# Kernel optimization log

Hardware: AMD Instinct MI355X
Metric: run time of the kernel (lower is better)

The kernel has to match this reference:

```python
import jax, jax.numpy as jnp
import numpy as np

KH = KW = 21          # kernel_size
DIL = 1               # dilation
Q_SCALE = 1e10        # floor-quantization scale from the original module


def setup_inputs() -> dict:
    key = jax.random.key(0)
    # (B, N, C, H, W) with N = num_input = 2
    inputs = jax.random.normal(key, (4, 2, 128, 128, 128), dtype=jnp.float32)
    return {"inputs": inputs}


def reference(inputs):
    B, N, C, H, W = inputs.shape
    Rh, Rw = (KH // 2) * DIL, (KW // 2) * DIL  # max displacement per axis

    # floor quantization with straight-through gradient (matches detach trick)
    s = jnp.float32(Q_SCALE)
    q = jax.lax.stop_gradient(jnp.floor(inputs * s) / s - inputs) + inputs

    src = q[:, :-1]        # (B, N-1, C, H, W)
    target = q[:, -1]      # (B, C, H, W)

    # zero padding == grid_sample padding_mode='zeros', nearest + integer offsets
    tp = jnp.pad(target, ((0, 0), (0, 0), (Rh, Rh), (Rw, Rw)))

    # row-major enumeration of displacements (dy, dx); slice start = R + d
    dy = jnp.arange(KH, dtype=jnp.int32) * DIL   # 0 .. 2*Rh
    dx = jnp.arange(KW, dtype=jnp.int32) * DIL
    starts = jnp.stack(jnp.meshgrid(dy, dx, indexing='ij'), axis=-1).reshape(-1, 2)  # (K, 2)

    def step(carry, st):
        # shifted[h, w] = target[h + dy, w + dx] with zeros outside
        sh = jax.lax.dynamic_slice(tp, (0, 0, st[0], st[1]), (B, C, H, W))
        # elementwise multiply + channel mean -> (B, N-1, H, W)
        return carry, jnp.mean(src * sh[:, None], axis=-3)

    _, ys = jax.lax.scan(step, None, starts)          # (K, B, N-1, H, W)
    out = jnp.moveaxis(ys, 0, 1)                      # (B, K, N-1, H, W)
    return out.reshape(B, KH * KW * (N - 1), H, W)    # stack dim=1 then flatten(1,2)
```

## Files before the change

kernel.cpp:

```cpp
#include <hip/hip_runtime.h>

#define HH 128
#define WW 128
#define CCH 128
#define NKD 21
#define RAD 10
#define HPAD 148
#define ROWH 40
#define CH_HALVES (148 * ROWH)
#define CH_BYTES  (CH_HALVES * 2)
#define IMG_HALVES (4 * CH_HALVES)

typedef _Float16 f16x8 __attribute__((ext_vector_type(8)));
typedef float    f32x4 __attribute__((ext_vector_type(4)));
typedef __fp16   h2f   __attribute__((ext_vector_type(2)));

union PK { uint4 u; h2f h[4]; };

__global__ __launch_bounds__(256)
void pack_tgt(const float* __restrict__ in, __fp16* __restrict__ img) {
    int n = blockIdx.x;
    int b = n / HPAD, i = n - b * HPAD;
    int tid = threadIdx.x;
    uint4* gi = (uint4*)(img + (size_t)n * IMG_HALVES);
    if (i < RAD || i > 137) {
        uint4 z = make_uint4(0, 0, 0, 0);
#pragma unroll
        for (int k = 0; k < 11; ++k) gi[k * 256 + tid] = z;
        if (tid < 144) gi[11 * 256 + tid] = z;
        return;
    }
    __shared__ __align__(16) char sraw[4 * CH_BYTES];
    {
        uint4 z = make_uint4(0, 0, 0, 0);
        uint4* sp = (uint4*)sraw;
#pragma unroll
        for (int k = 0; k < 11; ++k) sp[k * 256 + tid] = z;
        if (tid < 144) sp[11 * 256 + tid] = z;
    }
    __syncthreads();
    const float* tg = in + (size_t)(b * 2 + 1) * CCH * HH * WW + (size_t)(i - RAD) * WW;
    int w = tid & 127, half = tid >> 7;
    int p = w + RAD;
#pragma unroll
    for (int c2 = 0; c2 < 2; ++c2) {
        int cc = half * 2 + c2;
#pragma unroll
        for (int g = 0; g < 4; ++g) {
            float v[8];
#pragma unroll
            for (int j = 0; j < 8; ++j)
                v[j] = tg[(size_t)(cc * 32 + g * 8 + j) * (HH * WW) + w];
            PK q;
            q.h[0] = __builtin_amdgcn_cvt_pkrtz(v[0], v[1]);
            q.h[1] = __builtin_amdgcn_cvt_pkrtz(v[2], v[3]);
            q.h[2] = __builtin_amdgcn_cvt_pkrtz(v[4], v[5]);
            q.h[3] = __builtin_amdgcn_cvt_pkrtz(v[6], v[7]);
            *(uint4*)(sraw + (size_t)cc * CH_BYTES + p * 80 + g * 16) = q.u;
        }
    }
    __syncthreads();
    const uint4* si = (const uint4*)sraw;
#pragma unroll
    for (int k = 0; k < 11; ++k) gi[k * 256 + tid] = si[k * 256 + tid];
    if (tid < 144) gi[11 * 256 + tid] = si[11 * 256 + tid];
}

__global__ __launch_bounds__(256, 2)
void corr_mfma(const float* __restrict__ in, const __fp16* __restrict__ img_tgt,
               float* __restrict__ out) {
    int n = blockIdx.x;
    int xcd = n & 7, idx = n >> 3;
    int u = xcd * 64 + idx;
    int d = u & 1;
    int hpair = u >> 1;
    int b = hpair >> 6;
    int h0 = (hpair & 63) << 1;

    __shared__ __align__(16) char smem[4 * CH_BYTES + 25600];
    char*   s_ring = smem;
    __fp16* s_srch = (__fp16*)(smem + 4 * CH_BYTES);
    float*  s_o    = (float*)(smem + 4 * CH_BYTES);

    int tid = threadIdx.x;
    int q = tid >> 6, lane = tid & 63, r = lane & 15, g = lane >> 4;

    const __fp16* tgb = img_tgt + (size_t)(b * HPAD) * IMG_HALVES;
    const int hbase = h0 + d * 11;

    auto stage = [&](int t) {
        const uint4* gp = (const uint4*)(tgb + ((size_t)(hbase + (t >> 2)) * 4 + (t & 3)) * CH_HALVES)
                          + q * 185 + lane;
        char* lb = s_ring + (size_t)(t & 3) * CH_BYTES + q * 2960;
        __builtin_amdgcn_global_load_lds(
            (const __attribute__((address_space(1))) void*)gp,
            (__attribute__((address_space(3))) void*)lb, 16, 0, 0);
        __builtin_amdgcn_global_load_lds(
            (const __attribute__((address_space(1))) void*)(gp + 64),
            (__attribute__((address_space(3))) void*)(lb + 1024), 16, 0, 0);
        if (lane < 57)
            __builtin_amdgcn_global_load_lds(
                (const __attribute__((address_space(1))) void*)(gp + 128),
                (__attribute__((address_space(3))) void*)(lb + 2048), 16, 0, 0);
    };

    stage(0);
    stage(1);

    f16x8 a[2][2][4];
#pragma unroll
    for (int row = 0; row < 2; ++row) {
        const float* src = in + (size_t)(b * 2) * CCH * HH * WW + (size_t)(h0 + row) * WW;
        const float sc = 1.f / 128.f;
        int w = tid & 127, hb = tid >> 7;
#pragma unroll
        for (int chalf = 0; chalf < 2; ++chalf) {
#pragma unroll
            for (int i4 = 0; i4 < 4; ++i4) {
                int t4 = hb * 4 + i4;
                float v[8];
#pragma unroll
                for (int j = 0; j < 8; ++j)
                    v[j] = src[(size_t)(chalf * 64 + t4 * 8 + j) * (HH * WW) + w] * sc;
                PK qq;
                qq.h[0] = __builtin_amdgcn_cvt_pkrtz(v[0], v[1]);
                qq.h[1] = __builtin_amdgcn_cvt_pkrtz(v[2], v[3]);
                qq.h[2] = __builtin_amdgcn_cvt_pkrtz(v[4], v[5]);
                qq.h[3] = __builtin_amdgcn_cvt_pkrtz(v[6], v[7]);
                int slot = t4 ^ (w & 7);
                *(uint4*)&s_srch[w * 64 + slot * 8] = qq.u;
            }
            __syncthreads();
#pragma unroll
            for (int wi = 0; wi < 2; ++wi) {
                int wrow = (2 * q + wi) * 16 + r;
#pragma unroll
                for (int ksl = 0; ksl < 2; ++ksl) {
                    int slot = (ksl * 4 + g) ^ (wrow & 7);
                    a[row][wi][chalf * 2 + ksl] = *(const f16x8*)&s_srch[wrow * 64 + slot * 8];
                }
            }
            asm volatile("s_waitcnt lgkmcnt(0)" ::: "memory");
            __syncthreads();
        }
    }

    float* outb = out + (size_t)b * (NKD * NKD) * (HH * WW) + (size_t)h0 * WW;
    float* so = s_o + q * (32 * 50);

    for (int phl = 0; phl < 11; ++phl) {
        int ph_g = d * 11 + phl;
        int row0_on = (ph_g <= 20);
        int row1_on = (ph_g >= 1);

        f32x4 acc[2][2][3];
#pragma unroll
        for (int row = 0; row < 2; ++row)
#pragma unroll
            for (int wi = 0; wi < 2; ++wi)
#pragma unroll
                for (int pj = 0; pj < 3; ++pj)
#pragma unroll
                    for (int j = 0; j < 4; ++j) acc[row][wi][pj][j] = 0.f;

#pragma unroll
        for (int cc = 0; cc < 4; ++cc) {
            int t = phl * 4 + cc;
            if (cc < 2) {
                if (d == 0 && phl == 1) asm volatile("s_waitcnt vmcnt(6)" ::: "memory");
                else                    asm volatile("s_waitcnt vmcnt(9)" ::: "memory");
            } else if (t == 43) {
                asm volatile("s_waitcnt vmcnt(0)" ::: "memory");
            } else {
                asm volatile("s_waitcnt vmcnt(3)" ::: "memory");
            }
            __builtin_amdgcn_s_barrier();
            __builtin_amdgcn_sched_barrier(0);
            if (t + 2 < 44) stage(t + 2);

            const char* buf = s_ring + (size_t)(t & 3) * CH_BYTES;
            f16x8 bfr[4];
#pragma unroll
            for (int pi = 0; pi < 4; ++pi)
                bfr[pi] = *(const f16x8*)(buf + ((2 * q + pi) * 16 + r) * 80 + g * 16);

            if (row0_on) {
#pragma unroll
                for (int wi = 0; wi < 2; ++wi)
#pragma unroll
                    for (int pj = 0; pj < 3; ++pj)
                        acc[0][wi][pj] = __builtin_amdgcn_mfma_f32_16x16x32_f16(
                            a[0][wi][cc], bfr[wi + pj], acc[0][wi][pj], 0, 0, 0);
            }
            if (row1_on) {
#pragma unroll
                for (int wi = 0; wi < 2; ++wi)
#pragma unroll
                    for (int pj = 0; pj < 3; ++pj)
                        acc[1][wi][pj] = __builtin_amdgcn_mfma_f32_16x16x32_f16(
                            a[1][wi][cc], bfr[wi + pj], acc[1][wi][pj], 0, 0, 0);
            }
        }

#pragma unroll
        for (int row = 0; row < 2; ++row) {
            int dy = ph_g - row;
            if ((row == 0 && !row0_on) || (row == 1 && !row1_on)) continue;
#pragma unroll
            for (int wi = 0; wi < 2; ++wi)
#pragma unroll
                for (int pj = 0; pj < 3; ++pj)
#pragma unroll
                    for (int j = 0; j < 4; ++j)
                        so[(wi * 16 + 4 * g + j) * 50 + pj * 16 + r] = acc[row][wi][pj][j];
            asm volatile("s_waitcnt lgkmcnt(0)" ::: "memory");
            __builtin_amdgcn_sched_barrier(0);
            float* op = outb + (size_t)row * WW + (size_t)dy * NKD * (HH * WW);
#pragma unroll
            for (int k = 0; k < 3; ++k) {
                int f = k * 64 + lane;
                if (f < NKD * 8) {
                    int dx = f >> 3, w4l = (f & 7) << 2;
                    float4 v;
                    v.x = so[(w4l + 0) * 50 + ((w4l + 0) & 15) + dx];
                    v.y = so[(w4l + 1) * 50 + ((w4l + 1) & 15) + dx];
                    v.z = so[(w4l + 2) * 50 + ((w4l + 2) & 15) + dx];
                    v.w = so[(w4l + 3) * 50 + ((w4l + 3) & 15) + dx];
                    *(float4*)&op[(size_t)dx * (HH * WW) + q * 32 + w4l] = v;
                }
            }
            asm volatile("s_waitcnt lgkmcnt(0)" ::: "memory");
        }
    }
}

extern "C" void kernel_launch(void* const* d_in, const int* in_sizes, int n_in,
                              void* d_out, int out_size, void* d_ws, size_t ws_size,
                              hipStream_t stream) {
    const float* in = (const float*)d_in[0];
    float* out = (float*)d_out;
    __fp16* img_tgt = (__fp16*)d_ws;

    hipLaunchKernelGGL(pack_tgt, dim3(4 * HPAD), dim3(256), 0, stream, in, img_tgt);
    hipLaunchKernelGGL(corr_mfma, dim3(512), dim3(256), 0, stream, in, img_tgt, out);
}
```

Before: 57.13 us.

## Replace LDS ring staging of target tiles with direct register double-buffered global loads

Target B-fragments are no longer staged through a 4-deep LDS ring with async global_load_lds, waitcnt and per-step barriers. Each lane now loads its four fragments straight from global memory into a two-slot register buffer, prefetching the chunk two steps ahead. This removes the per-chunk barriers and cuts LDS usage, which may allow higher occupancy. The cost is uncoalesced 16-byte per-lane global loads with no shared reuse, and load latency must now be hidden by the register prefetch alone.

```diff
diff --git a/kernel.cpp b/kernel.cpp
--- a/kernel.cpp
+++ b/kernel.cpp
@@ -77,35 +77,15 @@
     int b = hpair >> 6;
     int h0 = (hpair & 63) << 1;
 
-    __shared__ __align__(16) char smem[4 * CH_BYTES + 25600];
-    char*   s_ring = smem;
-    __fp16* s_srch = (__fp16*)(smem + 4 * CH_BYTES);
-    float*  s_o    = (float*)(smem + 4 * CH_BYTES);
+    __shared__ __align__(16) char smem[25600];
+    __fp16* s_srch = (__fp16*)smem;
+    float*  s_o    = (float*)smem;
 
     int tid = threadIdx.x;
     int q = tid >> 6, lane = tid & 63, r = lane & 15, g = lane >> 4;
 
-    const __fp16* tgb = img_tgt + (size_t)(b * HPAD) * IMG_HALVES;
+    const char* tgbc = (const char*)(img_tgt + (size_t)(b * HPAD) * IMG_HALVES);
     const int hbase = h0 + d * 11;
-
-    auto stage = [&](int t) {
-        const uint4* gp = (const uint4*)(tgb + ((size_t)(hbase + (t >> 2)) * 4 + (t & 3)) * CH_HALVES)
-                          + q * 185 + lane;
-        char* lb = s_ring + (size_t)(t & 3) * CH_BYTES + q * 2960;
-        __builtin_amdgcn_global_load_lds(
-            (const __attribute__((address_space(1))) void*)gp,
-            (__attribute__((address_space(3))) void*)lb, 16, 0, 0);
-        __builtin_amdgcn_global_load_lds(
-            (const __attribute__((address_space(1))) void*)(gp + 64),
-            (__attribute__((address_space(3))) void*)(lb + 1024), 16, 0, 0);
-        if (lane < 57)
-            __builtin_amdgcn_global_load_lds(
-                (const __attribute__((address_space(1))) void*)(gp + 128),
-                (__attribute__((address_space(3))) void*)(lb + 2048), 16, 0, 0);
-    };
-
-    stage(0);
-    stage(1);
 
     f16x8 a[2][2][4];
 #pragma unroll
@@ -145,8 +125,26 @@
         }
     }
 
+    int off[4];
+#pragma unroll
+    for (int pi = 0; pi < 4; ++pi) {
+        int prow = (2 * q + pi) * 16 + r;
+        if (prow > 147) prow = 147;
+        off[pi] = prow * 80 + g * 16;
+    }
+
     float* outb = out + (size_t)b * (NKD * NKD) * (HH * WW) + (size_t)h0 * WW;
     float* so = s_o + q * (32 * 50);
+
+    uint4 buf[2][4];
+    {
+        const char* c0 = tgbc + ((size_t)hbase * 4 + 0) * CH_BYTES;
+        const char* c1 = tgbc + ((size_t)hbase * 4 + 1) * CH_BYTES;
+#pragma unroll
+        for (int pi = 0; pi < 4; ++pi) buf[0][pi] = *(const uint4*)(c0 + off[pi]);
+#pragma unroll
+        for (int pi = 0; pi < 4; ++pi) buf[1][pi] = *(const uint4*)(c1 + off[pi]);
+    }
 
     for (int phl = 0; phl < 11; ++phl) {
         int ph_g = d * 11 + phl;
@@ -166,23 +164,18 @@
 #pragma unroll
         for (int cc = 0; cc < 4; ++cc) {
             int t = phl * 4 + cc;
-            if (cc < 2) {
-                if (d == 0 && phl == 1) asm volatile("s_waitcnt vmcnt(6)" ::: "memory");
-                else                    asm volatile("s_waitcnt vmcnt(9)" ::: "memory");
-            } else if (t == 43) {
-                asm volatile("s_waitcnt vmcnt(0)" ::: "memory");
-            } else {
-                asm volatile("s_waitcnt vmcnt(3)" ::: "memory");
-            }
-            __builtin_amdgcn_s_barrier();
-            __builtin_amdgcn_sched_barrier(0);
-            if (t + 2 < 44) stage(t + 2);
-
-            const char* buf = s_ring + (size_t)(t & 3) * CH_BYTES;
             f16x8 bfr[4];
 #pragma unroll
             for (int pi = 0; pi < 4; ++pi)
-                bfr[pi] = *(const f16x8*)(buf + ((2 * q + pi) * 16 + r) * 80 + g * 16);
+                bfr[pi] = __builtin_bit_cast(f16x8, buf[cc & 1][pi]);
+
+            if (t + 2 < 44) {
+                const char* cp = tgbc
+                    + ((size_t)(hbase + ((t + 2) >> 2)) * 4 + ((t + 2) & 3)) * CH_BYTES;
+#pragma unroll
+                for (int pi = 0; pi < 4; ++pi)
+                    buf[cc & 1][pi] = *(const uint4*)(cp + off[pi]);
+            }
 
             if (row0_on) {
 #pragma unroll
```

Result: faster. 54.61 us (-4.4%).
